# Kernel optimization log

Hardware: AMD Instinct MI355X
Metric: run time of the kernel (lower is better)

## Reference

```python
import jax, jax.numpy as jnp
import numpy as np

B, S, D, A_DIM = 8, 2048, 256, 64

def setup_inputs() -> dict:
    key = jax.random.key(0)
    k_x, k_wm, k_wl, k_eps = jax.random.split(key, 4)
    return {
        "x": jax.random.normal(k_x, (B, S, D), dtype=jnp.float32),
        "W_mean": jax.random.normal(k_wm, (D, A_DIM), dtype=jnp.float32) * (1.0 / np.sqrt(D)),
        "b_mean": jnp.zeros((A_DIM,), dtype=jnp.float32),
        "W_logvar": jax.random.normal(k_wl, (D, A_DIM), dtype=jnp.float32) * (1.0 / np.sqrt(D)),
        "b_logvar": jnp.zeros((A_DIM,), dtype=jnp.float32),
        "eps": jax.random.normal(k_eps, (B, S, A_DIM), dtype=jnp.float32),
    }

def reference(x, W_mean, b_mean, W_logvar, b_logvar, eps):
    d = x.shape[-1]
    scale = 1.0 / jnp.sqrt(jnp.asarray(d, dtype=x.dtype))
    # S_det = x x^T / sqrt(d)  -> [B, S, S]
    scores = jnp.einsum("bsd,btd->bst", x, x) * scale
    attn = jax.nn.softmax(scores, axis=-1)
    # A_det = softmax(S) x  -> [B, S, D]
    A_det = jnp.einsum("bst,btd->bsd", attn, x)
    A_mean = A_det @ W_mean + b_mean        # [B, S, A_DIM]
    A_logvar = A_det @ W_logvar + b_logvar  # [B, S, A_DIM]
    A = A_mean + jnp.exp(0.5 * A_logvar) * eps  # sqrt(exp(logvar)) = exp(logvar/2)
    return (A_mean, A_logvar, A)
```

## Files before the change

### kernel.cpp

```cpp
#include <hip/hip_runtime.h>

#define B_ 8
#define S_ 2048
#define D_ 256

typedef _Float16 f16;
typedef f16 f16x2 __attribute__((ext_vector_type(2)));
typedef f16 f16x8 __attribute__((ext_vector_type(8)));
typedef float f32x16 __attribute__((ext_vector_type(16)));
typedef unsigned int u32;
typedef u32 u32x4 __attribute__((ext_vector_type(4)));

typedef const __attribute__((address_space(1))) unsigned int* gptr_t;
typedef __attribute__((address_space(3))) unsigned int* lptr_t;

__device__ __forceinline__ void gload_lds16(const void* g, void* l) {
  __builtin_amdgcn_global_load_lds((gptr_t)(unsigned long long)g,
                                   (lptr_t)(unsigned long long)l, 16, 0, 0);
}

__device__ __forceinline__ u32 packf16(float a, float b) {
  f16x2 t; t[0] = (f16)a; t[1] = (f16)b;
  return __builtin_bit_cast(u32, t);
}

__device__ __forceinline__ void pack16(const f32x16& p, int hi, u32x4& o0, u32x4& o1) {
#pragma unroll
  for (int c2 = 0; c2 < 2; ++c2) {
    u32 a1 = packf16(p[8 * c2 + 0], p[8 * c2 + 1]);
    u32 a2 = packf16(p[8 * c2 + 2], p[8 * c2 + 3]);
    u32 b1 = packf16(p[8 * c2 + 4], p[8 * c2 + 5]);
    u32 b2 = packf16(p[8 * c2 + 6], p[8 * c2 + 7]);
    u32 xa1 = __shfl_xor(a1, 32), xa2 = __shfl_xor(a2, 32);
    u32 xb1 = __shfl_xor(b1, 32), xb2 = __shfl_xor(b2, 32);
    u32x4 f;
    f[0] = hi ? xb1 : a1;
    f[1] = hi ? xb2 : a2;
    f[2] = hi ? b1 : xa1;
    f[3] = hi ? b2 : xa2;
    if (c2) o1 = f; else o0 = f;
  }
}

#define SC2F 0.09016844f
#define NMAXR 20.0f

__global__ void prep(const float* __restrict__ x, const float* __restrict__ Wm,
                     const float* __restrict__ Wl, f16* __restrict__ xh,
                     f16* __restrict__ xt, float* __restrict__ n2,
                     f16* __restrict__ Wt) {
  __shared__ f16 tile[64][264];
  const int bid = blockIdx.x;
  const int t = threadIdx.x;
  if (bid < 256) {
    const int b = bid >> 5, st = bid & 31;
    const int s0 = st * 64;
    const float* xb = x + ((size_t)(b * S_ + s0)) * D_;
    f16* xhb = xh + ((size_t)(b * S_ + s0)) * D_;
#pragma unroll
    for (int it = 0; it < 16; ++it) {
      int flat = it * 256 + t;
      int r = flat >> 6, c4 = flat & 63;
      float4 v = *reinterpret_cast<const float4*>(xb + r * 256 + c4 * 4);
      f16 h0 = (f16)v.x, h1 = (f16)v.y, h2 = (f16)v.z, h3 = (f16)v.w;
      f16x2 p0 = {h0, h1}, p1 = {h2, h3};
      uint2 wv; wv.x = __builtin_bit_cast(u32, p0); wv.y = __builtin_bit_cast(u32, p1);
      *reinterpret_cast<uint2*>(xhb + r * 256 + c4 * 4) = wv;
      tile[r][c4 * 4 + 0] = h0; tile[r][c4 * 4 + 1] = h1;
      tile[r][c4 * 4 + 2] = h2; tile[r][c4 * 4 + 3] = h3;
    }
    __syncthreads();
    {
      int r = t >> 2, qd = t & 3;
      float s = 0.0f;
#pragma unroll
      for (int i = 0; i < 8; ++i) {
        f16x8 v = *reinterpret_cast<const f16x8*>(&tile[r][qd * 64 + i * 8]);
#pragma unroll
        for (int u = 0; u < 8; ++u) { float f = (float)v[u]; s += f * f; }
      }
      s += __shfl_xor(s, 1); s += __shfl_xor(s, 2);
      if (qd == 0) n2[b * S_ + s0 + r] = s;
    }
    {
      f16* xtb = xt + ((size_t)(b * D_ + t)) * S_ + s0;
#pragma unroll
      for (int s8 = 0; s8 < 8; ++s8) {
        f16x8 ov;
#pragma unroll
        for (int u = 0; u < 8; ++u) ov[u] = tile[s8 * 8 + u][t];
        *reinterpret_cast<f16x8*>(xtb + s8 * 8) = ov;
      }
    }
  } else {
    int idx = (bid - 256) * 1024 + t * 4;
    int j = idx >> 8, d = idx & 255;
#pragma unroll
    for (int k2 = 0; k2 < 4; ++k2) {
      float v = (j < 64) ? Wm[(d + k2) * 64 + j] : Wl[(d + k2) * 64 + (j - 64)];
      Wt[idx + k2] = (f16)v;
    }
  }
}

__launch_bounds__(512, 4)
__global__ void gemm1_kern(const f16* __restrict__ xh, const float* __restrict__ n2,
                           f16* __restrict__ P, float* __restrict__ Lp,
                           int b0, int bm, int bsh) {
  __shared__ f16 Aq[2][8192];
  __shared__ f16 Bk[2][8192];
  const int idx = blockIdx.x;
  const int bl = idx & bm;
  const int kt = (idx >> bsh) & 15;
  const int qt = idx >> (bsh + 4);
  const int b = b0 + bl;
  const int qb = qt * 128, kb = kt * 128;
  const int tid = threadIdx.x, lane = tid & 63, w = tid >> 6;
  const int l31 = lane & 31, hi = lane >> 5;
  const int wq = w >> 2, wk = w & 3;
  const f16* xb = xh + (size_t)b * S_ * D_;

#define G1_STAGE(st, pp)                                                       \
  { _Pragma("unroll") for (int i = 0; i < 4; ++i) {                            \
      int ii = w * 4 + i;                                                      \
      int flat = ii * 64 + lane;                                               \
      bool isB = ii >= 16;                                                     \
      int ch = isB ? flat - 1024 : flat;                                       \
      int r = ch >> 3, c = ch & 7;                                             \
      int csrc = c ^ (r & 7);                                                  \
      const f16* src = xb + (size_t)((isB ? kb : qb) + r) * 256 +              \
                       (st) * 64 + csrc * 8;                                   \
      f16* dst = (isB ? &Bk[pp][0] : &Aq[pp][0]) + ch * 8;                     \
      gload_lds16(src, dst);                                                   \
    } }

  f32x16 acc[2];
#pragma unroll
  for (int i = 0; i < 2; ++i)
#pragma unroll
    for (int e = 0; e < 16; ++e) acc[i][e] = 0.0f;

  G1_STAGE(0, 0);
  __syncthreads();
#pragma unroll
  for (int t = 0; t < 4; ++t) {
    const int p = t & 1;
    if (t < 3) G1_STAGE(t + 1, p ^ 1);
#pragma unroll
    for (int kc = 0; kc < 4; ++kc) {
      int cc = ((2 * kc + hi) ^ (l31 & 7)) * 8;
      f16x8 af  = *reinterpret_cast<const f16x8*>(&Bk[p][(wk * 32 + l31) * 64 + cc]);
      f16x8 bf0 = *reinterpret_cast<const f16x8*>(&Aq[p][(wq * 64 + l31) * 64 + cc]);
      f16x8 bf1 = *reinterpret_cast<const f16x8*>(&Aq[p][(wq * 64 + 32 + l31) * 64 + cc]);
      acc[0] = __builtin_amdgcn_mfma_f32_32x32x16_f16(af, bf0, acc[0], 0, 0, 0);
      acc[1] = __builtin_amdgcn_mfma_f32_32x32x16_f16(af, bf1, acc[1], 0, 0, 0);
    }
    __syncthreads();
  }
#undef G1_STAGE

  float r2[2], lsum[2];
  int qrow[2];
#pragma unroll
  for (int ni = 0; ni < 2; ++ni) {
    qrow[ni] = qb + wq * 64 + ni * 32 + l31;
    r2[ni] = sqrtf(n2[b * S_ + qrow[ni]]) * (NMAXR * SC2F);
    lsum[ni] = 0.0f;
  }
#pragma unroll
  for (int ni = 0; ni < 2; ++ni)
#pragma unroll
    for (int j = 0; j < 16; ++j) {
      float v = exp2f(acc[ni][j] * SC2F - r2[ni]);
      acc[ni][j] = v;
      lsum[ni] += v;
    }
#pragma unroll
  for (int ni = 0; ni < 2; ++ni) lsum[ni] += __shfl_xor(lsum[ni], 32);

  const int colb = kb + wk * 32;
#pragma unroll
  for (int ni = 0; ni < 2; ++ni) {
    u32x4 s0, s1;
    pack16(acc[ni], hi, s0, s1);
    size_t rowp = (size_t)(bl * S_ + qrow[ni]) * 2048;
    *reinterpret_cast<u32x4*>(P + rowp + colb + hi * 8) = s0;
    *reinterpret_cast<u32x4*>(P + rowp + colb + 16 + hi * 8) = s1;
  }

  float* Lred = (float*)(&Aq[0][0]);
  if (hi == 0) {
    Lred[(wq * 64 + l31) * 4 + wk] = lsum[0];
    Lred[(wq * 64 + 32 + l31) * 4 + wk] = lsum[1];
  }
  __syncthreads();
  if (tid < 128) {
    float s = Lred[tid * 4] + Lred[tid * 4 + 1] + Lred[tid * 4 + 2] + Lred[tid * 4 + 3];
    Lp[(size_t)(bl * 16 + kt) * 2048 + qb + tid] = s;
  }
}

__launch_bounds__(512, 6)
__global__ void gemm2_kern(const f16* __restrict__ P, const f16* __restrict__ xt,
                           const float* __restrict__ Lp, f16* __restrict__ adet,
                           int b0, int bm, int bsh) {
  __shared__ f16 Pt[2][8192];
  __shared__ f16 Xt[2][4096];
  const int idx = blockIdx.x;
  const int bl = idx & bm;
  const int dt = (idx >> bsh) & 3;
  const int qt = idx >> (bsh + 2);
  const int b = b0 + bl;
  const int qb = qt * 128, db = dt * 64;
  const int tid = threadIdx.x, lane = tid & 63, w = tid >> 6;
  const int l31 = lane & 31, hi = lane >> 5;
  const int wq = w >> 1, wd = w & 1;
  const f16* xtb = xt + (size_t)b * D_ * S_;

#define G2_STAGE(st, pp)                                                       \
  { _Pragma("unroll") for (int i = 0; i < 3; ++i) {                            \
      int ii = w * 3 + i;                                                      \
      int flat = ii * 64 + lane;                                               \
      bool isX = ii >= 16;                                                     \
      int ch = isX ? flat - 1024 : flat;                                       \
      int r = ch >> 3, c = ch & 7;                                             \
      int csrc = c ^ (r & 7);                                                  \
      const f16* src = isX                                                     \
          ? xtb + (size_t)(db + r) * 2048 + (st) * 64 + csrc * 8               \
          : P + (size_t)(bl * S_ + qb + r) * 2048 + (st) * 64 + csrc * 8;      \
      f16* dst = (isX ? &Xt[pp][0] : &Pt[pp][0]) + ch * 8;                     \
      gload_lds16(src, dst);                                                   \
    } }

  f32x16 acc;
#pragma unroll
  for (int e = 0; e < 16; ++e) acc[e] = 0.0f;

  G2_STAGE(0, 0);
  __syncthreads();
#pragma unroll 1
  for (int t = 0; t < 32; ++t) {
    const int p = t & 1;
    if (t < 31) G2_STAGE(t + 1, p ^ 1);
#pragma unroll
    for (int kc = 0; kc < 4; ++kc) {
      int cc = ((2 * kc + hi) ^ (l31 & 7)) * 8;
      f16x8 af = *reinterpret_cast<const f16x8*>(&Xt[p][(wd * 32 + l31) * 64 + cc]);
      f16x8 bf = *reinterpret_cast<const f16x8*>(&Pt[p][(wq * 32 + l31) * 64 + cc]);
      acc = __builtin_amdgcn_mfma_f32_32x32x16_f16(af, bf, acc, 0, 0, 0);
    }
    __syncthreads();
  }
#undef G2_STAGE

  const int q = qb + wq * 32 + l31;
  float L = 0.0f;
#pragma unroll
  for (int kt = 0; kt < 16; ++kt) L += Lp[(size_t)(bl * 16 + kt) * 2048 + q];
  float rL = 1.0f / L;
#pragma unroll
  for (int e = 0; e < 16; ++e) acc[e] *= rL;
  u32x4 s0, s1;
  pack16(acc, hi, s0, s1);
  f16* arow = adet + (size_t)(b * S_ + q) * 256 + db + wd * 32;
  *reinterpret_cast<u32x4*>(arow + hi * 8) = s0;
  *reinterpret_cast<u32x4*>(arow + 16 + hi * 8) = s1;
}

__launch_bounds__(64)
__global__ void proj_kern(const f16* __restrict__ adet, const f16* __restrict__ Wt,
                          const float* __restrict__ bm, const float* __restrict__ bl,
                          const float* __restrict__ eps, float* __restrict__ out) {
  const int lane = threadIdx.x & 63;
  const int l31 = lane & 31, hi = lane >> 5;
  const int rb = blockIdx.x * 32;
  f16x8 af[16];
  const f16* arow = adet + (size_t)(rb + l31) * 256;
#pragma unroll
  for (int kk = 0; kk < 16; ++kk)
    af[kk] = *reinterpret_cast<const f16x8*>(arow + kk * 16 + hi * 8);
  f32x16 acc[4];
#pragma unroll
  for (int i = 0; i < 4; ++i)
#pragma unroll
    for (int j = 0; j < 16; ++j) acc[i][j] = 0.0f;
#pragma unroll
  for (int ns = 0; ns < 4; ++ns) {
    const f16* wrow = Wt + (size_t)(l31 + 32 * ns) * 256;
#pragma unroll
    for (int kk = 0; kk < 16; ++kk) {
      f16x8 bf = *reinterpret_cast<const f16x8*>(wrow + kk * 16 + hi * 8);
      acc[ns] = __builtin_amdgcn_mfma_f32_32x32x16_f16(af[kk], bf, acc[ns], 0, 0, 0);
    }
  }
#pragma unroll
  for (int ns = 0; ns < 2; ++ns) {
    int c = l31 + 32 * ns;
    float bmv = bm[c], blv = bl[c];
#pragma unroll
    for (int r = 0; r < 16; ++r) {
      int row = (r & 3) + 8 * (r >> 2) + 4 * hi;
      int grow = rb + row;
      float mean = acc[ns][r] + bmv;
      float lv = acc[ns + 2][r] + blv;
      float e = eps[grow * 64 + c];
      float a = mean + exp2f(0.7213475204f * lv) * e;
      out[grow * 64 + c] = mean;
      out[1048576 + grow * 64 + c] = lv;
      out[2097152 + grow * 64 + c] = a;
    }
  }
}

extern "C" void kernel_launch(void* const* d_in, const int* in_sizes, int n_in,
                              void* d_out, int out_size, void* d_ws, size_t ws_size,
                              hipStream_t stream) {
  (void)in_sizes; (void)n_in; (void)out_size;
  const float* x   = (const float*)d_in[0];
  const float* Wm  = (const float*)d_in[1];
  const float* bmv = (const float*)d_in[2];
  const float* Wl  = (const float*)d_in[3];
  const float* blv = (const float*)d_in[4];
  const float* ep  = (const float*)d_in[5];
  float* out = (float*)d_out;

  char* ws = (char*)d_ws;
  f16*   xh   = (f16*)(ws + 0);
  f16*   xt   = (f16*)(ws + 8388608);
  f16*   adet = (f16*)(ws + 16777216);
  f16*   Wt   = (f16*)(ws + 25165824);
  float* n2   = (float*)(ws + 25231360);
  float* Lp   = (float*)(ws + 25296896);
  const size_t P_off = 26345472;
  f16*   Pbuf = (f16*)(ws + P_off);

  int bpp = 1;
  if      (ws_size >= P_off + (size_t)8 * 2048 * 2048 * 2) bpp = 8;
  else if (ws_size >= P_off + (size_t)4 * 2048 * 2048 * 2) bpp = 4;
  else if (ws_size >= P_off + (size_t)2 * 2048 * 2048 * 2) bpp = 2;
  const int bsh = (bpp == 8) ? 3 : (bpp == 4) ? 2 : (bpp == 2) ? 1 : 0;
  const int bm = bpp - 1;

  prep<<<288, 256, 0, stream>>>(x, Wm, Wl, xh, xt, n2, Wt);
  for (int b0 = 0; b0 < 8; b0 += bpp) {
    gemm1_kern<<<bpp * 256, 512, 0, stream>>>(xh, n2, Pbuf, Lp, b0, bm, bsh);
    gemm2_kern<<<bpp * 64, 512, 0, stream>>>(Pbuf, xt, Lp, adet, b0, bm, bsh);
  }
  proj_kern<<<512, 64, 0, stream>>>(adet, Wt, bmv, blv, ep, out);
}
```

Baseline: 83.17 us.

## Retile both attention GEMMs and add a 4-stage pipeline with raw barriers to gemm2

gemm1 now computes 128x256 tiles per block with a 2x2 MFMA grid per wave and a 32-wide K step over 8 iterations. This raises register reuse and halves the number of blocks and the Lp partial count. gemm2 moves to 256-thread blocks with 64x128 output tiles and a 4-buffer LDS ring driven by explicit vmcnt waits and raw s_barrier, so global loads can stay in flight across iterations. proj_kern remaps block indices to spread rows across batches. The trade-offs are higher register pressure, fewer blocks in flight, and the risk of getting the hand-written waitcnt accounting wrong.

```diff
diff --git a/kernel.cpp b/kernel.cpp
--- a/kernel.cpp
+++ b/kernel.cpp
@@ -22,6 +22,12 @@
 __device__ __forceinline__ u32 packf16(float a, float b) {
   f16x2 t; t[0] = (f16)a; t[1] = (f16)b;
   return __builtin_bit_cast(u32, t);
+}
+
+__device__ __forceinline__ void barrier_raw() {
+  __builtin_amdgcn_sched_barrier(0);
+  __builtin_amdgcn_s_barrier();
+  __builtin_amdgcn_sched_barrier(0);
 }
 
 __device__ __forceinline__ void pack16(const f32x16& p, int hi, u32x4& o0, u32x4& o1) {
@@ -44,6 +50,7 @@
 
 #define SC2F 0.09016844f
 #define NMAXR 20.0f
+#define SWZ(r, s) ((s) ^ ((r) & 3) ^ (((r) >> 2) & 3))
 
 __global__ void prep(const float* __restrict__ x, const float* __restrict__ Wm,
                      const float* __restrict__ Wl, f16* __restrict__ xh,
@@ -107,57 +114,64 @@
 __global__ void gemm1_kern(const f16* __restrict__ xh, const float* __restrict__ n2,
                            f16* __restrict__ P, float* __restrict__ Lp,
                            int b0, int bm, int bsh) {
-  __shared__ f16 Aq[2][8192];
+  __shared__ f16 Aq[2][4096];
   __shared__ f16 Bk[2][8192];
   const int idx = blockIdx.x;
   const int bl = idx & bm;
-  const int kt = (idx >> bsh) & 15;
-  const int qt = idx >> (bsh + 4);
+  const int kt = (idx >> bsh) & 7;
+  const int qt = idx >> (bsh + 3);
   const int b = b0 + bl;
-  const int qb = qt * 128, kb = kt * 128;
+  const int qb = qt * 128, kb = kt * 256;
   const int tid = threadIdx.x, lane = tid & 63, w = tid >> 6;
   const int l31 = lane & 31, hi = lane >> 5;
   const int wq = w >> 2, wk = w & 3;
   const f16* xb = xh + (size_t)b * S_ * D_;
 
 #define G1_STAGE(st, pp)                                                       \
-  { _Pragma("unroll") for (int i = 0; i < 4; ++i) {                            \
-      int ii = w * 4 + i;                                                      \
-      int flat = ii * 64 + lane;                                               \
-      bool isB = ii >= 16;                                                     \
-      int ch = isB ? flat - 1024 : flat;                                       \
-      int r = ch >> 3, c = ch & 7;                                             \
-      int csrc = c ^ (r & 7);                                                  \
-      const f16* src = xb + (size_t)((isB ? kb : qb) + r) * 256 +              \
-                       (st) * 64 + csrc * 8;                                   \
-      f16* dst = (isB ? &Bk[pp][0] : &Aq[pp][0]) + ch * 8;                     \
-      gload_lds16(src, dst);                                                   \
+  {                                                                            \
+    { int c = tid; int r = c >> 2, sl = c & 3; int cs = SWZ(r, sl);            \
+      gload_lds16(xb + (size_t)(qb + r) * 256 + (st) * 32 + cs * 8,            \
+                  &Aq[pp][0] + c * 8); }                                       \
+    _Pragma("unroll") for (int i = 0; i < 2; ++i) {                            \
+      int c = i * 512 + tid; int r = c >> 2, sl = c & 3; int cs = SWZ(r, sl);  \
+      gload_lds16(xb + (size_t)(kb + r) * 256 + (st) * 32 + cs * 8,            \
+                  &Bk[pp][0] + c * 8); }                                       \
+  }
+
+#define G1_COMP(pp)                                                           \
+  { _Pragma("unroll") for (int kc = 0; kc < 2; ++kc) {                        \
+      int s = kc * 2 + hi;                                                    \
+      f16x8 af[2], bf[2];                                                     \
+      _Pragma("unroll") for (int mi = 0; mi < 2; ++mi) {                      \
+        int row = wk * 64 + mi * 32 + l31;                                    \
+        af[mi] = *reinterpret_cast<const f16x8*>(&Bk[pp][row * 32 + SWZ(row, s) * 8]); } \
+      _Pragma("unroll") for (int ni = 0; ni < 2; ++ni) {                      \
+        int row = wq * 64 + ni * 32 + l31;                                    \
+        bf[ni] = *reinterpret_cast<const f16x8*>(&Aq[pp][row * 32 + SWZ(row, s) * 8]); } \
+      _Pragma("unroll") for (int mi = 0; mi < 2; ++mi)                        \
+        _Pragma("unroll") for (int ni = 0; ni < 2; ++ni)                      \
+          acc[mi][ni] = __builtin_amdgcn_mfma_f32_32x32x16_f16(af[mi], bf[ni], acc[mi][ni], 0, 0, 0); \
     } }
 
-  f32x16 acc[2];
+  f32x16 acc[2][2];
 #pragma unroll
   for (int i = 0; i < 2; ++i)
 #pragma unroll
-    for (int e = 0; e < 16; ++e) acc[i][e] = 0.0f;
+    for (int j = 0; j < 2; ++j)
+#pragma unroll
+      for (int e = 0; e < 16; ++e) acc[i][j][e] = 0.0f;
 
   G1_STAGE(0, 0);
   __syncthreads();
-#pragma unroll
-  for (int t = 0; t < 4; ++t) {
+#pragma unroll 1
+  for (int t = 0; t < 8; ++t) {
     const int p = t & 1;
-    if (t < 3) G1_STAGE(t + 1, p ^ 1);
-#pragma unroll
-    for (int kc = 0; kc < 4; ++kc) {
-      int cc = ((2 * kc + hi) ^ (l31 & 7)) * 8;
-      f16x8 af  = *reinterpret_cast<const f16x8*>(&Bk[p][(wk * 32 + l31) * 64 + cc]);
-      f16x8 bf0 = *reinterpret_cast<const f16x8*>(&Aq[p][(wq * 64 + l31) * 64 + cc]);
-      f16x8 bf1 = *reinterpret_cast<const f16x8*>(&Aq[p][(wq * 64 + 32 + l31) * 64 + cc]);
-      acc[0] = __builtin_amdgcn_mfma_f32_32x32x16_f16(af, bf0, acc[0], 0, 0, 0);
-      acc[1] = __builtin_amdgcn_mfma_f32_32x32x16_f16(af, bf1, acc[1], 0, 0, 0);
-    }
+    if (t < 7) G1_STAGE(t + 1, p ^ 1);
+    G1_COMP(p);
     __syncthreads();
   }
 #undef G1_STAGE
+#undef G1_COMP
 
   float r2[2], lsum[2];
   int qrow[2];
@@ -168,25 +182,29 @@
     lsum[ni] = 0.0f;
   }
 #pragma unroll
-  for (int ni = 0; ni < 2; ++ni)
-#pragma unroll
-    for (int j = 0; j < 16; ++j) {
-      float v = exp2f(acc[ni][j] * SC2F - r2[ni]);
-      acc[ni][j] = v;
-      lsum[ni] += v;
-    }
+  for (int mi = 0; mi < 2; ++mi)
+#pragma unroll
+    for (int ni = 0; ni < 2; ++ni)
+#pragma unroll
+      for (int j = 0; j < 16; ++j) {
+        float v = exp2f(acc[mi][ni][j] * SC2F - r2[ni]);
+        acc[mi][ni][j] = v;
+        lsum[ni] += v;
+      }
 #pragma unroll
   for (int ni = 0; ni < 2; ++ni) lsum[ni] += __shfl_xor(lsum[ni], 32);
 
-  const int colb = kb + wk * 32;
-#pragma unroll
-  for (int ni = 0; ni < 2; ++ni) {
-    u32x4 s0, s1;
-    pack16(acc[ni], hi, s0, s1);
-    size_t rowp = (size_t)(bl * S_ + qrow[ni]) * 2048;
-    *reinterpret_cast<u32x4*>(P + rowp + colb + hi * 8) = s0;
-    *reinterpret_cast<u32x4*>(P + rowp + colb + 16 + hi * 8) = s1;
-  }
+#pragma unroll
+  for (int mi = 0; mi < 2; ++mi)
+#pragma unroll
+    for (int ni = 0; ni < 2; ++ni) {
+      u32x4 s0, s1;
+      pack16(acc[mi][ni], hi, s0, s1);
+      size_t rowp = (size_t)(bl * S_ + qrow[ni]) * 2048;
+      int colb = kb + wk * 64 + mi * 32;
+      *reinterpret_cast<u32x4*>(P + rowp + colb + hi * 8) = s0;
+      *reinterpret_cast<u32x4*>(P + rowp + colb + 16 + hi * 8) = s1;
+    }
 
   float* Lred = (float*)(&Aq[0][0]);
   if (hi == 0) {
@@ -196,75 +214,91 @@
   __syncthreads();
   if (tid < 128) {
     float s = Lred[tid * 4] + Lred[tid * 4 + 1] + Lred[tid * 4 + 2] + Lred[tid * 4 + 3];
-    Lp[(size_t)(bl * 16 + kt) * 2048 + qb + tid] = s;
-  }
-}
-
-__launch_bounds__(512, 6)
+    Lp[(size_t)(bl * 8 + kt) * 2048 + qb + tid] = s;
+  }
+}
+
+__launch_bounds__(256, 3)
 __global__ void gemm2_kern(const f16* __restrict__ P, const f16* __restrict__ xt,
                            const float* __restrict__ Lp, f16* __restrict__ adet,
                            int b0, int bm, int bsh) {
-  __shared__ f16 Pt[2][8192];
-  __shared__ f16 Xt[2][4096];
+  __shared__ f16 Pt[4][2048];
+  __shared__ f16 Xt[4][4096];
   const int idx = blockIdx.x;
   const int bl = idx & bm;
-  const int dt = (idx >> bsh) & 3;
-  const int qt = idx >> (bsh + 2);
+  const int dt = (idx >> bsh) & 1;
+  const int qt = idx >> (bsh + 1);
   const int b = b0 + bl;
-  const int qb = qt * 128, db = dt * 64;
+  const int qb = qt * 64, db = dt * 128;
   const int tid = threadIdx.x, lane = tid & 63, w = tid >> 6;
   const int l31 = lane & 31, hi = lane >> 5;
-  const int wq = w >> 1, wd = w & 1;
+  const int wq = w & 1, wd = w >> 1;
   const f16* xtb = xt + (size_t)b * D_ * S_;
 
-#define G2_STAGE(st, pp)                                                       \
-  { _Pragma("unroll") for (int i = 0; i < 3; ++i) {                            \
-      int ii = w * 3 + i;                                                      \
-      int flat = ii * 64 + lane;                                               \
-      bool isX = ii >= 16;                                                     \
-      int ch = isX ? flat - 1024 : flat;                                       \
-      int r = ch >> 3, c = ch & 7;                                             \
-      int csrc = c ^ (r & 7);                                                  \
-      const f16* src = isX                                                     \
-          ? xtb + (size_t)(db + r) * 2048 + (st) * 64 + csrc * 8               \
-          : P + (size_t)(bl * S_ + qb + r) * 2048 + (st) * 64 + csrc * 8;      \
-      f16* dst = (isX ? &Xt[pp][0] : &Pt[pp][0]) + ch * 8;                     \
-      gload_lds16(src, dst);                                                   \
-    } }
-
-  f32x16 acc;
-#pragma unroll
-  for (int e = 0; e < 16; ++e) acc[e] = 0.0f;
+#define G2_STAGE(tt, tb)                                                       \
+  {                                                                            \
+    { int c = tid; int r = c >> 2, sl = c & 3; int cs = SWZ(r, sl);            \
+      gload_lds16(P + (size_t)(bl * S_ + qb + r) * 2048 + (tt) * 32 + cs * 8,  \
+                  &Pt[tb][0] + c * 8); }                                       \
+    _Pragma("unroll") for (int i = 0; i < 2; ++i) {                            \
+      int c = i * 256 + tid; int r = c >> 2, sl = c & 3; int cs = SWZ(r, sl);  \
+      gload_lds16(xtb + (size_t)(db + r) * 2048 + (tt) * 32 + cs * 8,          \
+                  &Xt[tb][0] + c * 8); }                                       \
+  }
+
+#define G2_COMP(tb)                                                           \
+  { _Pragma("unroll") for (int kc = 0; kc < 2; ++kc) {                        \
+      int s = kc * 2 + hi;                                                    \
+      int qrow = wq * 32 + l31;                                               \
+      f16x8 bf = *reinterpret_cast<const f16x8*>(&Pt[tb][qrow * 32 + SWZ(qrow, s) * 8]); \
+      _Pragma("unroll") for (int ni = 0; ni < 2; ++ni) {                      \
+        int drow = wd * 64 + ni * 32 + l31;                                   \
+        f16x8 af = *reinterpret_cast<const f16x8*>(&Xt[tb][drow * 32 + SWZ(drow, s) * 8]); \
+        acc[ni] = __builtin_amdgcn_mfma_f32_32x32x16_f16(af, bf, acc[ni], 0, 0, 0); \
+      } } }
+
+  f32x16 acc[2];
+#pragma unroll
+  for (int i = 0; i < 2; ++i)
+#pragma unroll
+    for (int e = 0; e < 16; ++e) acc[i][e] = 0.0f;
 
   G2_STAGE(0, 0);
-  __syncthreads();
+  G2_STAGE(1, 1);
+  G2_STAGE(2, 2);
 #pragma unroll 1
-  for (int t = 0; t < 32; ++t) {
-    const int p = t & 1;
-    if (t < 31) G2_STAGE(t + 1, p ^ 1);
-#pragma unroll
-    for (int kc = 0; kc < 4; ++kc) {
-      int cc = ((2 * kc + hi) ^ (l31 & 7)) * 8;
-      f16x8 af = *reinterpret_cast<const f16x8*>(&Xt[p][(wd * 32 + l31) * 64 + cc]);
-      f16x8 bf = *reinterpret_cast<const f16x8*>(&Pt[p][(wq * 32 + l31) * 64 + cc]);
-      acc = __builtin_amdgcn_mfma_f32_32x32x16_f16(af, bf, acc, 0, 0, 0);
-    }
-    __syncthreads();
-  }
+  for (int t = 0; t < 62; ++t) {
+    asm volatile("s_waitcnt vmcnt(6)" ::: "memory");
+    barrier_raw();
+    if (t < 61) G2_STAGE(t + 3, (t + 3) & 3);
+    G2_COMP(t & 3);
+  }
+  asm volatile("s_waitcnt vmcnt(3)" ::: "memory");
+  barrier_raw();
+  G2_COMP(2);
+  asm volatile("s_waitcnt vmcnt(0)" ::: "memory");
+  barrier_raw();
+  G2_COMP(3);
 #undef G2_STAGE
+#undef G2_COMP
 
   const int q = qb + wq * 32 + l31;
   float L = 0.0f;
 #pragma unroll
-  for (int kt = 0; kt < 16; ++kt) L += Lp[(size_t)(bl * 16 + kt) * 2048 + q];
+  for (int kt = 0; kt < 8; ++kt) L += Lp[(size_t)(bl * 8 + kt) * 2048 + q];
   float rL = 1.0f / L;
 #pragma unroll
-  for (int e = 0; e < 16; ++e) acc[e] *= rL;
-  u32x4 s0, s1;
-  pack16(acc, hi, s0, s1);
-  f16* arow = adet + (size_t)(b * S_ + q) * 256 + db + wd * 32;
-  *reinterpret_cast<u32x4*>(arow + hi * 8) = s0;
-  *reinterpret_cast<u32x4*>(arow + 16 + hi * 8) = s1;
+  for (int ni = 0; ni < 2; ++ni)
+#pragma unroll
+    for (int e = 0; e < 16; ++e) acc[ni][e] *= rL;
+#pragma unroll
+  for (int ni = 0; ni < 2; ++ni) {
+    u32x4 s0, s1;
+    pack16(acc[ni], hi, s0, s1);
+    f16* arow = adet + (size_t)(b * S_ + q) * 256 + db + wd * 64 + ni * 32;
+    *reinterpret_cast<u32x4*>(arow + hi * 8) = s0;
+    *reinterpret_cast<u32x4*>(arow + 16 + hi * 8) = s1;
+  }
 }
 
 __launch_bounds__(64)
@@ -273,7 +307,8 @@
                           const float* __restrict__ eps, float* __restrict__ out) {
   const int lane = threadIdx.x & 63;
   const int l31 = lane & 31, hi = lane >> 5;
-  const int rb = blockIdx.x * 32;
+  const int bidx = blockIdx.x;
+  const int rb = ((bidx & 7) * 64 + (bidx >> 3)) * 32;
   f16x8 af[16];
   const f16* arow = adet + (size_t)(rb + l31) * 256;
 #pragma unroll
@@ -331,7 +366,7 @@
   f16*   Wt   = (f16*)(ws + 25165824);
   float* n2   = (float*)(ws + 25231360);
   float* Lp   = (float*)(ws + 25296896);
-  const size_t P_off = 26345472;
+  const size_t P_off = 25821184;
   f16*   Pbuf = (f16*)(ws + P_off);
 
   int bpp = 1;
@@ -343,8 +378,8 @@
 
   prep<<<288, 256, 0, stream>>>(x, Wm, Wl, xh, xt, n2, Wt);
   for (int b0 = 0; b0 < 8; b0 += bpp) {
-    gemm1_kern<<<bpp * 256, 512, 0, stream>>>(xh, n2, Pbuf, Lp, b0, bm, bsh);
-    gemm2_kern<<<bpp * 64, 512, 0, stream>>>(Pbuf, xt, Lp, adet, b0, bm, bsh);
+    gemm1_kern<<<bpp * 128, 512, 0, stream>>>(xh, n2, Pbuf, Lp, b0, bm, bsh);
+    gemm2_kern<<<bpp * 64, 256, 0, stream>>>(Pbuf, xt, Lp, adet, b0, bm, bsh);
   }
   proj_kern<<<512, 64, 0, stream>>>(adet, Wt, bmv, blv, ep, out);
 }
```

After: 89.81 us. +8.0%, slower.

## Exploit score symmetry: compute upper-triangular tiles and write transposed P tiles

Applied to the files above, without the earlier changes.

Because x·xᵀ is symmetric, gemm1 now launches only the 136 upper-triangular 128x128 tiles per batch instead of 256. Each off-diagonal tile also stages its raw scores in shared memory, recomputes the exponentials with the key row's normalizer, and writes the transposed P tile and its partial row sums. This roughly halves the MFMA and x-load work in gemm1, at the cost of an extra shared-memory transpose pass, more exp work and more synchronization in the epilogue. proj_kern's block-to-row mapping is also permuted.

```diff
diff --git a/kernel.cpp b/kernel.cpp
--- a/kernel.cpp
+++ b/kernel.cpp
@@ -44,6 +44,7 @@
 
 #define SC2F 0.09016844f
 #define NMAXR 20.0f
+#define SWZ(r, s) ((s) ^ ((r) & 3) ^ (((r) >> 2) & 3))
 
 __global__ void prep(const float* __restrict__ x, const float* __restrict__ Wm,
                      const float* __restrict__ Wl, f16* __restrict__ xh,
@@ -107,12 +108,16 @@
 __global__ void gemm1_kern(const f16* __restrict__ xh, const float* __restrict__ n2,
                            f16* __restrict__ P, float* __restrict__ Lp,
                            int b0, int bm, int bsh) {
-  __shared__ f16 Aq[2][8192];
-  __shared__ f16 Bk[2][8192];
+  __shared__ __align__(16) char smem[65536];
+  f16* Aq = (f16*)smem;
+  f16* Bk = (f16*)(smem + 32768);
   const int idx = blockIdx.x;
   const int bl = idx & bm;
-  const int kt = (idx >> bsh) & 15;
-  const int qt = idx >> (bsh + 4);
+  int tdec = idx >> bsh;
+  int qt = 0;
+#pragma unroll 1
+  while (tdec >= 16 - qt) { tdec -= 16 - qt; ++qt; }
+  const int kt = qt + tdec;
   const int b = b0 + bl;
   const int qb = qt * 128, kb = kt * 128;
   const int tid = threadIdx.x, lane = tid & 63, w = tid >> 6;
@@ -130,7 +135,7 @@
       int csrc = c ^ (r & 7);                                                  \
       const f16* src = xb + (size_t)((isB ? kb : qb) + r) * 256 +              \
                        (st) * 64 + csrc * 8;                                   \
-      f16* dst = (isB ? &Bk[pp][0] : &Aq[pp][0]) + ch * 8;                     \
+      f16* dst = (isB ? Bk : Aq) + ((pp) * 8192) + ch * 8;                     \
       gload_lds16(src, dst);                                                   \
     } }
 
@@ -149,15 +154,27 @@
 #pragma unroll
     for (int kc = 0; kc < 4; ++kc) {
       int cc = ((2 * kc + hi) ^ (l31 & 7)) * 8;
-      f16x8 af  = *reinterpret_cast<const f16x8*>(&Bk[p][(wk * 32 + l31) * 64 + cc]);
-      f16x8 bf0 = *reinterpret_cast<const f16x8*>(&Aq[p][(wq * 64 + l31) * 64 + cc]);
-      f16x8 bf1 = *reinterpret_cast<const f16x8*>(&Aq[p][(wq * 64 + 32 + l31) * 64 + cc]);
+      f16x8 af  = *reinterpret_cast<const f16x8*>(Bk + p * 8192 + (wk * 32 + l31) * 64 + cc);
+      f16x8 bf0 = *reinterpret_cast<const f16x8*>(Aq + p * 8192 + (wq * 64 + l31) * 64 + cc);
+      f16x8 bf1 = *reinterpret_cast<const f16x8*>(Aq + p * 8192 + (wq * 64 + 32 + l31) * 64 + cc);
       acc[0] = __builtin_amdgcn_mfma_f32_32x32x16_f16(af, bf0, acc[0], 0, 0, 0);
       acc[1] = __builtin_amdgcn_mfma_f32_32x32x16_f16(af, bf1, acc[1], 0, 0, 0);
     }
     __syncthreads();
   }
 #undef G1_STAGE
+
+  float* raw = (float*)smem;
+  if (kt != qt) {
+#pragma unroll
+    for (int ni = 0; ni < 2; ++ni)
+#pragma unroll
+      for (int j = 0; j < 16; ++j) {
+        int kvloc = wk * 32 + (j & 3) + 8 * (j >> 2) + 4 * hi;
+        int qloc = wq * 64 + ni * 32 + l31;
+        raw[kvloc * 128 + (qloc ^ ((kvloc & 7) << 2))] = acc[ni][j];
+      }
+  }
 
   float r2[2], lsum[2];
   int qrow[2];
@@ -188,7 +205,40 @@
     *reinterpret_cast<u32x4*>(P + rowp + colb + 16 + hi * 8) = s1;
   }
 
-  float* Lred = (float*)(&Aq[0][0]);
+  if (kt != qt) {
+    __syncthreads();
+    const int kvr = tid >> 2;
+    const int qseg = (tid & 3) * 32;
+    float r2kv = sqrtf(n2[b * S_ + kb + kvr]) * (NMAXR * SC2F);
+    u32 ow[16];
+    float tsum = 0.0f;
+#pragma unroll
+    for (int c8 = 0; c8 < 8; ++c8) {
+      int qs = qseg + c8 * 4;
+      float4 v = *reinterpret_cast<const float4*>(
+          &raw[kvr * 128 + (qs ^ ((kvr & 7) << 2))]);
+      float e0 = exp2f(v.x * SC2F - r2kv), e1 = exp2f(v.y * SC2F - r2kv);
+      float e2 = exp2f(v.z * SC2F - r2kv), e3 = exp2f(v.w * SC2F - r2kv);
+      tsum += (e0 + e1) + (e2 + e3);
+      ow[c8 * 2 + 0] = packf16(e0, e1);
+      ow[c8 * 2 + 1] = packf16(e2, e3);
+    }
+    size_t rowp = (size_t)(bl * S_ + kb + kvr) * 2048;
+#pragma unroll
+    for (int sseg = 0; sseg < 4; ++sseg) {
+      u32x4 sv;
+      sv[0] = ow[sseg * 4 + 0]; sv[1] = ow[sseg * 4 + 1];
+      sv[2] = ow[sseg * 4 + 2]; sv[3] = ow[sseg * 4 + 3];
+      *reinterpret_cast<u32x4*>(P + rowp + qb + qseg + sseg * 8) = sv;
+    }
+    tsum += __shfl_xor(tsum, 1);
+    tsum += __shfl_xor(tsum, 2);
+    if ((tid & 3) == 0)
+      Lp[(size_t)(bl * 16 + qt) * 2048 + kb + kvr] = tsum;
+  }
+
+  __syncthreads();
+  float* Lred = (float*)smem;
   if (hi == 0) {
     Lred[(wq * 64 + l31) * 4 + wk] = lsum[0];
     Lred[(wq * 64 + 32 + l31) * 4 + wk] = lsum[1];
@@ -226,9 +276,9 @@
       int r = ch >> 3, c = ch & 7;                                             \
       int csrc = c ^ (r & 7);                                                  \
       const f16* src = isX                                                     \
-          ? xtb + (size_t)(db + r) * 2048 + (st) * 64 + csrc * 8               \
-          : P + (size_t)(bl * S_ + qb + r) * 2048 + (st) * 64 + csrc * 8;      \
-      f16* dst = (isX ? &Xt[pp][0] : &Pt[pp][0]) + ch * 8;                     \
+          ? xtb + (size_t)(db + r) * 2048 + ((st) * 64) + csrc * 8             \
+          : P + (size_t)(bl * S_ + qb + r) * 2048 + ((st) * 64) + csrc * 8;    \
+      f16* dst = (isX ? &Xt[(pp)][0] : &Pt[(pp)][0]) + ch * 8;                 \
       gload_lds16(src, dst);                                                   \
     } }
 
@@ -273,7 +323,8 @@
                           const float* __restrict__ eps, float* __restrict__ out) {
   const int lane = threadIdx.x & 63;
   const int l31 = lane & 31, hi = lane >> 5;
-  const int rb = blockIdx.x * 32;
+  const int bidx = blockIdx.x;
+  const int rb = ((bidx & 7) * 64 + (bidx >> 3)) * 32;
   f16x8 af[16];
   const f16* arow = adet + (size_t)(rb + l31) * 256;
 #pragma unroll
@@ -343,7 +394,7 @@
 
   prep<<<288, 256, 0, stream>>>(x, Wm, Wl, xh, xt, n2, Wt);
   for (int b0 = 0; b0 < 8; b0 += bpp) {
-    gemm1_kern<<<bpp * 256, 512, 0, stream>>>(xh, n2, Pbuf, Lp, b0, bm, bsh);
+    gemm1_kern<<<bpp * 136, 512, 0, stream>>>(xh, n2, Pbuf, Lp, b0, bm, bsh);
     gemm2_kern<<<bpp * 64, 512, 0, stream>>>(Pbuf, xt, Lp, adet, b0, bm, bsh);
   }
   proj_kern<<<512, 64, 0, stream>>>(adet, Wt, bmv, blv, ep, out);
```

New measurement: 83.55 us. No clear change (+0.4%).
